# Kernel optimization log

Measured on AMD Instinct MI355X. Metric: run time of the kernel, lower is better.

Reference implementation:

```python
import jax, jax.numpy as jnp
import numpy as np

B, S, D = 4, 2048, 1024
E = 8
H = int(D * 2.5)  # 2560


def setup_inputs() -> dict:
    key = jax.random.key(0)
    ks = jax.random.split(key, 6)
    scale = 0.02
    x = jax.random.normal(ks[0], (B, S, D), dtype=jnp.float32)
    Wr = jax.random.normal(ks[1], (E, D), dtype=jnp.float32) * scale   # router: logits = x @ Wr.T
    Wg = jax.random.normal(ks[2], (E, H, D), dtype=jnp.float32) * scale  # gate proj per expert
    Wu = jax.random.normal(ks[3], (E, H, D), dtype=jnp.float32) * scale  # up proj per expert
    Wd = jax.random.normal(ks[4], (E, D, H), dtype=jnp.float32) * scale  # down proj per expert
    return {"x": x, "Wr": Wr, "Wg": Wg, "Wu": Wu, "Wd": Wd, "top_k": 2}


def reference(x, Wr, Wg, Wu, Wd, top_k):
    num_experts = Wg.shape[0]
    logits = jnp.einsum('bsd,ed->bse', x, Wr)              # [B,S,E]
    probs = jax.nn.softmax(logits, axis=-1)
    k = min(top_k, num_experts)
    topv, topi = jax.lax.top_k(probs, k)                   # [B,S,k]
    out = jnp.zeros_like(x)
    for ei in range(num_experts):
        mask = jnp.any(topi == ei, axis=-1)                # [B,S] bool
        h = jax.nn.silu(jnp.einsum('bsd,hd->bsh', x, Wg[ei])) \
            * jnp.einsum('bsd,hd->bsh', x, Wu[ei])         # [B,S,H]
        ex = jnp.einsum('bsh,dh->bsd', h, Wd[ei])          # [B,S,D]
        w = (probs[..., ei] * mask.astype(x.dtype))[..., None]
        out = out + ex * w
    return (out, logits, probs, topi)
```

## Files before the change

kernel.cpp:

```cpp
#include <hip/hip_runtime.h>

#define T_TOK 8192
#define DD    1024
#define EE    8
#define HH    2560
#define PAIR_CAP (T_TOK*2 + 128)
#define MT_MAX 64
#define NT1   (HH/64)
#define NT2   (DD/128)

typedef __attribute__((ext_vector_type(8))) short bf16x8;
typedef __attribute__((ext_vector_type(4))) float f32x4;

__device__ __forceinline__ unsigned short f2b(float f) {
  union { float f; unsigned u; } v; v.f = f;
  unsigned r = v.u + 0x7FFFu + ((v.u >> 16) & 1u);
  return (unsigned short)(r >> 16);
}

__device__ __forceinline__ void async16(const void* g, void* l) {
  __builtin_amdgcn_global_load_lds(
      (const __attribute__((address_space(1))) unsigned int*)(unsigned long long)g,
      (__attribute__((address_space(3))) unsigned int*)l,
      16, 0, 0);
}

__global__ void zero_f4(float4* p, int n4) {
  int i = blockIdx.x * blockDim.x + threadIdx.x;
  if (i < n4) p[i] = make_float4(0.f, 0.f, 0.f, 0.f);
}

__global__ void zero_ints(int* a, int n) {
  int i = threadIdx.x;
  if (i < n) a[i] = 0;
}

__global__ void conv_bf16(const float* __restrict__ s, unsigned short* __restrict__ d, int n4) {
  int i = blockIdx.x * blockDim.x + threadIdx.x;
  if (i >= n4) return;
  float4 v = ((const float4*)s)[i];
  ushort4 o;
  o.x = f2b(v.x); o.y = f2b(v.y); o.z = f2b(v.z); o.w = f2b(v.w);
  ((ushort4*)d)[i] = o;
}

__global__ __launch_bounds__(256) void router(
    const float* __restrict__ x, const float* __restrict__ Wr,
    float* __restrict__ o_logits, float* __restrict__ o_probs, float* __restrict__ o_topi,
    int* __restrict__ top_e, float* __restrict__ top_p, int* __restrict__ counts)
{
  __shared__ float sWr[EE * DD];
  int tid = threadIdx.x;
  const float4* w4 = (const float4*)Wr;
  float4* s4 = (float4*)sWr;
  for (int i = tid; i < EE * DD / 4; i += 256) s4[i] = w4[i];
  __syncthreads();

  int wv = tid >> 6, lane = tid & 63;
  int t = blockIdx.x * 4 + wv;
  const float* xt = x + (size_t)t * DD;

  float acc[EE];
#pragma unroll
  for (int e = 0; e < EE; e++) acc[e] = 0.f;
  for (int d = lane; d < DD; d += 64) {
    float xv = xt[d];
#pragma unroll
    for (int e = 0; e < EE; e++) acc[e] += xv * sWr[e * DD + d];
  }
#pragma unroll
  for (int e = 0; e < EE; e++) {
#pragma unroll
    for (int off = 32; off; off >>= 1) acc[e] += __shfl_down(acc[e], off);
  }
  if (lane == 0) {
    float mx = acc[0];
#pragma unroll
    for (int e = 1; e < EE; e++) mx = fmaxf(mx, acc[e]);
    float p[EE]; float sum = 0.f;
#pragma unroll
    for (int e = 0; e < EE; e++) { p[e] = __expf(acc[e] - mx); sum += p[e]; }
    float inv = 1.f / sum;
#pragma unroll
    for (int e = 0; e < EE; e++) {
      p[e] *= inv;
      o_logits[(size_t)t * EE + e] = acc[e];
      o_probs [(size_t)t * EE + e] = p[e];
    }
    int i0 = 0;
#pragma unroll
    for (int e = 1; e < EE; e++) if (p[e] > p[i0]) i0 = e;
    int i1 = (i0 == 0) ? 1 : 0;
#pragma unroll
    for (int e = 0; e < EE; e++) if (e != i0 && p[e] > p[i1]) i1 = e;

    o_topi[t * 2 + 0] = (float)i0;
    o_topi[t * 2 + 1] = (float)i1;
    top_e[t * 2 + 0] = i0; top_e[t * 2 + 1] = i1;
    top_p[t * 2 + 0] = p[i0]; top_p[t * 2 + 1] = p[i1];
    atomicAdd(&counts[i0], 1);
    atomicAdd(&counts[i1], 1);
  }
}

__global__ void mk_offsets(const int* __restrict__ counts, int* __restrict__ offsets,
                           int* __restrict__ cursors) {
  if (threadIdx.x == 0) {
    int s = 0;
    for (int e = 0; e < EE; e++) { offsets[e] = s; s += counts[e]; }
  }
  if (threadIdx.x < EE) cursors[threadIdx.x] = 0;
}

__global__ void scatter(const int* __restrict__ top_e, const float* __restrict__ top_p,
                        const int* __restrict__ offsets, int* __restrict__ cursors,
                        int* __restrict__ list, float* __restrict__ wl) {
  int t = blockIdx.x * blockDim.x + threadIdx.x;
  if (t >= T_TOK) return;
#pragma unroll
  for (int k = 0; k < 2; k++) {
    int e = top_e[t * 2 + k];
    int pos = atomicAdd(&cursors[e], 1);
    int dst = offsets[e] + pos;
    list[dst] = t;
    wl[dst] = top_p[t * 2 + k];
  }
}

__global__ __launch_bounds__(256) void gemm_gateup(
    const unsigned short* __restrict__ xb,
    const unsigned short* __restrict__ Wgb,
    const unsigned short* __restrict__ Wub,
    const int* __restrict__ list, const int* __restrict__ offsets,
    const int* __restrict__ counts,
    unsigned short* __restrict__ hbuf)
{
  int bx = blockIdx.x;
  int e = bx / (MT_MAX * NT1);
  int rem = bx - e * (MT_MAX * NT1);
  int mt = rem / NT1;
  int nt = rem - mt * NT1;
  int n_e = counts[e];
  if (mt * 128 >= n_e) return;
  int off_e = offsets[e];

  __shared__ unsigned short sA [128 * 32];
  __shared__ unsigned short sBg[ 64 * 32];
  __shared__ unsigned short sBu[ 64 * 32];

  int tid = threadIdx.x, wv = tid >> 6, lane = tid & 63;
  const unsigned short* wg_e = Wgb + (size_t)e * HH * DD;
  const unsigned short* wu_e = Wub + (size_t)e * HH * DD;

  size_t aBase[2];
#pragma unroll
  for (int i = 0; i < 2; i++) {
    int c = i * 256 + tid;
    int r = c >> 2;
    int idx = mt * 128 + r;
    if (idx >= n_e) idx = n_e - 1;
    int tok = list[off_e + idx];
    aBase[i] = (size_t)tok * DD + (size_t)((c & 3) * 8);
  }
  int rB = tid >> 2;
  size_t bBase = (size_t)(nt * 64 + rB) * DD + (size_t)((tid & 3) * 8);

  f32x4 accg[4][2] = {};
  f32x4 accu[4][2] = {};
  int wm = (wv >> 1) * 64, wn = (wv & 1) * 32;
  unsigned short* ldsA0 = sA  + (wv * 64) * 8;
  unsigned short* ldsA1 = sA  + (256 + wv * 64) * 8;
  unsigned short* ldsBg = sBg + (wv * 64) * 8;
  unsigned short* ldsBu = sBu + (wv * 64) * 8;

  for (int k0 = 0; k0 < DD; k0 += 32) {
    __syncthreads();
    async16(xb + aBase[0] + k0, ldsA0);
    async16(xb + aBase[1] + k0, ldsA1);
    async16(wg_e + bBase + k0, ldsBg);
    async16(wu_e + bBase + k0, ldsBu);
    __syncthreads();

    bf16x8 af[4], bg[2], bu[2];
#pragma unroll
    for (int fi = 0; fi < 4; fi++)
      af[fi] = *(const bf16x8*)&sA[(wm + fi * 16 + (lane & 15)) * 32 + (lane >> 4) * 8];
#pragma unroll
    for (int fj = 0; fj < 2; fj++) {
      bg[fj] = *(const bf16x8*)&sBg[(wn + fj * 16 + (lane & 15)) * 32 + (lane >> 4) * 8];
      bu[fj] = *(const bf16x8*)&sBu[(wn + fj * 16 + (lane & 15)) * 32 + (lane >> 4) * 8];
    }
#pragma unroll
    for (int fi = 0; fi < 4; fi++)
#pragma unroll
      for (int fj = 0; fj < 2; fj++) {
        accg[fi][fj] = __builtin_amdgcn_mfma_f32_16x16x32_bf16(af[fi], bg[fj], accg[fi][fj], 0, 0, 0);
        accu[fi][fj] = __builtin_amdgcn_mfma_f32_16x16x32_bf16(af[fi], bu[fj], accu[fi][fj], 0, 0, 0);
      }
  }

#pragma unroll
  for (int fi = 0; fi < 4; fi++) {
    int mBase = mt * 128 + wm + fi * 16 + ((lane >> 4) << 2);
#pragma unroll
    for (int fj = 0; fj < 2; fj++) {
      int col = nt * 64 + wn + fj * 16 + (lane & 15);
#pragma unroll
      for (int r = 0; r < 4; r++) {
        int m = mBase + r;
        if (m < n_e) {
          float g = accg[fi][fj][r];
          float u = accu[fi][fj][r];
          float hv = g / (1.f + __expf(-g)) * u;
          hbuf[(size_t)(off_e + m) * HH + col] = f2b(hv);
        }
      }
    }
  }
}

__global__ __launch_bounds__(256) void gemm_down(
    const unsigned short* __restrict__ hbuf,
    const unsigned short* __restrict__ Wdb,
    const int* __restrict__ list, const int* __restrict__ offsets,
    const int* __restrict__ counts, const float* __restrict__ wl,
    float* __restrict__ out)
{
  int bx = blockIdx.x;
  int e = bx / (MT_MAX * NT2);
  int rem = bx - e * (MT_MAX * NT2);
  int mt = rem / NT2;
  int nt = rem - mt * NT2;
  int n_e = counts[e];
  if (mt * 128 >= n_e) return;
  int off_e = offsets[e];

  __shared__ unsigned short sA[128 * 32];
  __shared__ unsigned short sB[128 * 32];
  int tid = threadIdx.x, wv = tid >> 6, lane = tid & 63;
  const unsigned short* wd_e = Wdb + (size_t)e * DD * HH;

  size_t aBase[2], bBase[2];
#pragma unroll
  for (int i = 0; i < 2; i++) {
    int c = i * 256 + tid;
    int r = c >> 2;
    aBase[i] = (size_t)(off_e + mt * 128 + r) * HH + (size_t)((c & 3) * 8);
    bBase[i] = (size_t)(nt * 128 + r) * HH + (size_t)((c & 3) * 8);
  }

  f32x4 acc[4][4] = {};
  int wm = (wv >> 1) * 64, wn = (wv & 1) * 64;
  unsigned short* ldsA0 = sA + (wv * 64) * 8;
  unsigned short* ldsA1 = sA + (256 + wv * 64) * 8;
  unsigned short* ldsB0 = sB + (wv * 64) * 8;
  unsigned short* ldsB1 = sB + (256 + wv * 64) * 8;

  for (int k0 = 0; k0 < HH; k0 += 32) {
    __syncthreads();
    async16(hbuf + aBase[0] + k0, ldsA0);
    async16(hbuf + aBase[1] + k0, ldsA1);
    async16(wd_e + bBase[0] + k0, ldsB0);
    async16(wd_e + bBase[1] + k0, ldsB1);
    __syncthreads();

    bf16x8 af[4], bf[4];
#pragma unroll
    for (int f = 0; f < 4; f++) {
      af[f] = *(const bf16x8*)&sA[(wm + f * 16 + (lane & 15)) * 32 + (lane >> 4) * 8];
      bf[f] = *(const bf16x8*)&sB[(wn + f * 16 + (lane & 15)) * 32 + (lane >> 4) * 8];
    }
#pragma unroll
    for (int fi = 0; fi < 4; fi++)
#pragma unroll
      for (int fj = 0; fj < 4; fj++)
        acc[fi][fj] = __builtin_amdgcn_mfma_f32_16x16x32_bf16(af[fi], bf[fj], acc[fi][fj], 0, 0, 0);
  }

#pragma unroll
  for (int fi = 0; fi < 4; fi++) {
    int mBase = mt * 128 + wm + fi * 16 + ((lane >> 4) << 2);
#pragma unroll
    for (int r = 0; r < 4; r++) {
      int m = mBase + r;
      if (m < n_e) {
        int tok   = list[off_e + m];
        float wgt = wl[off_e + m];
        float* orow = out + (size_t)tok * DD + nt * 128 + wn;
#pragma unroll
        for (int fj = 0; fj < 4; fj++)
          atomicAdd(&orow[fj * 16 + (lane & 15)], acc[fi][fj][r] * wgt);
      }
    }
  }
}

extern "C" void kernel_launch(void* const* d_in, const int* in_sizes, int n_in,
                              void* d_out, int out_size, void* d_ws, size_t ws_size,
                              hipStream_t stream) {
  const float* x  = (const float*)d_in[0];
  const float* Wr = (const float*)d_in[1];
  const float* Wg = (const float*)d_in[2];
  const float* Wu = (const float*)d_in[3];
  const float* Wd = (const float*)d_in[4];

  float* out      = (float*)d_out;
  float* o_logits = out + (size_t)T_TOK * DD;
  float* o_probs  = o_logits + (size_t)T_TOK * EE;
  float* o_topi   = o_probs + (size_t)T_TOK * EE;

  char* w = (char*)d_ws;
  auto alloc = [&](size_t bytes) {
    char* p = w;
    w += (bytes + 255) & ~(size_t)255;
    return p;
  };
  unsigned short* Wgb = (unsigned short*)alloc((size_t)EE * HH * DD * 2);
  unsigned short* Wub = (unsigned short*)alloc((size_t)EE * HH * DD * 2);
  unsigned short* Wdb = (unsigned short*)alloc((size_t)EE * DD * HH * 2);
  unsigned short* xb  = (unsigned short*)alloc((size_t)T_TOK * DD * 2);
  unsigned short* hb  = (unsigned short*)alloc((size_t)PAIR_CAP * HH * 2);
  int*   top_e   = (int*)  alloc((size_t)T_TOK * 2 * 4);
  float* top_p   = (float*)alloc((size_t)T_TOK * 2 * 4);
  int*   counts  = (int*)  alloc(64);
  int*   offsets = (int*)  alloc(64);
  int*   cursors = (int*)  alloc(64);
  int*   list    = (int*)  alloc((size_t)PAIR_CAP * 4);
  float* wl      = (float*)alloc((size_t)PAIR_CAP * 4);

  zero_ints<<<1, 64, 0, stream>>>(counts, EE);
  {
    int n4 = T_TOK * DD / 4;
    zero_f4<<<(n4 + 255) / 256, 256, 0, stream>>>((float4*)out, n4);
  }
  {
    int nw4 = EE * HH * DD / 4;
    conv_bf16<<<(nw4 + 255) / 256, 256, 0, stream>>>(Wg, Wgb, nw4);
    conv_bf16<<<(nw4 + 255) / 256, 256, 0, stream>>>(Wu, Wub, nw4);
    conv_bf16<<<(nw4 + 255) / 256, 256, 0, stream>>>(Wd, Wdb, nw4);
    int nx4 = T_TOK * DD / 4;
    conv_bf16<<<(nx4 + 255) / 256, 256, 0, stream>>>(x, xb, nx4);
  }
  router<<<T_TOK / 4, 256, 0, stream>>>(x, Wr, o_logits, o_probs, o_topi, top_e, top_p, counts);
  mk_offsets<<<1, 64, 0, stream>>>(counts, offsets, cursors);
  scatter<<<T_TOK / 256, 256, 0, stream>>>(top_e, top_p, offsets, cursors, list, wl);
  gemm_gateup<<<EE * MT_MAX * NT1, 256, 0, stream>>>(xb, Wgb, Wub, list, offsets, counts, hb);
  gemm_down<<<EE * MT_MAX * NT2, 256, 0, stream>>>(hb, Wdb, list, offsets, counts, wl, out);
}
```

Before: 958.6 us.

## Use K=64 swizzled LDS tiles and replace atomic scatter with a combine pass

Both expert GEMMs now stage 64-wide K tiles in LDS using an XOR swizzle, which halves the number of barrier pairs per K step and is meant to reduce LDS bank conflicts. The down GEMM stores its per-pair results unweighted to a temporary buffer (aliased onto the no-longer-needed bf16 gate weights) instead of issuing float atomics into the output. A new combine kernel does the weighted sum of each token's two expert rows, so the output-zeroing pass can be dropped. This costs an extra round trip through a temporary buffer of pairs by D floats, and it relies on Wgb not being read after gemm_gateup.

```diff
diff --git a/kernel.cpp b/kernel.cpp
--- a/kernel.cpp
+++ b/kernel.cpp
@@ -23,11 +23,6 @@
       (const __attribute__((address_space(1))) unsigned int*)(unsigned long long)g,
       (__attribute__((address_space(3))) unsigned int*)l,
       16, 0, 0);
-}
-
-__global__ void zero_f4(float4* p, int n4) {
-  int i = blockIdx.x * blockDim.x + threadIdx.x;
-  if (i < n4) p[i] = make_float4(0.f, 0.f, 0.f, 0.f);
 }
 
 __global__ void zero_ints(int* a, int n) {
@@ -112,9 +107,9 @@
   if (threadIdx.x < EE) cursors[threadIdx.x] = 0;
 }
 
-__global__ void scatter(const int* __restrict__ top_e, const float* __restrict__ top_p,
+__global__ void scatter(const int* __restrict__ top_e,
                         const int* __restrict__ offsets, int* __restrict__ cursors,
-                        int* __restrict__ list, float* __restrict__ wl) {
+                        int* __restrict__ list, int* __restrict__ slot) {
   int t = blockIdx.x * blockDim.x + threadIdx.x;
   if (t >= T_TOK) return;
 #pragma unroll
@@ -123,7 +118,7 @@
     int pos = atomicAdd(&cursors[e], 1);
     int dst = offsets[e] + pos;
     list[dst] = t;
-    wl[dst] = top_p[t * 2 + k];
+    slot[t * 2 + k] = dst;
   }
 }
 
@@ -144,59 +139,74 @@
   if (mt * 128 >= n_e) return;
   int off_e = offsets[e];
 
-  __shared__ unsigned short sA [128 * 32];
-  __shared__ unsigned short sBg[ 64 * 32];
-  __shared__ unsigned short sBu[ 64 * 32];
+  __shared__ unsigned short sA [128 * 64];
+  __shared__ unsigned short sBg[ 64 * 64];
+  __shared__ unsigned short sBu[ 64 * 64];
 
   int tid = threadIdx.x, wv = tid >> 6, lane = tid & 63;
   const unsigned short* wg_e = Wgb + (size_t)e * HH * DD;
   const unsigned short* wu_e = Wub + (size_t)e * HH * DD;
 
-  size_t aBase[2];
-#pragma unroll
-  for (int i = 0; i < 2; i++) {
+  size_t aBase[4];
+#pragma unroll
+  for (int i = 0; i < 4; i++) {
     int c = i * 256 + tid;
-    int r = c >> 2;
+    int r = c >> 3, j = c & 7;
+    int jj = j ^ (r & 7);
     int idx = mt * 128 + r;
     if (idx >= n_e) idx = n_e - 1;
     int tok = list[off_e + idx];
-    aBase[i] = (size_t)tok * DD + (size_t)((c & 3) * 8);
-  }
-  int rB = tid >> 2;
-  size_t bBase = (size_t)(nt * 64 + rB) * DD + (size_t)((tid & 3) * 8);
+    aBase[i] = (size_t)tok * DD + (size_t)(jj * 8);
+  }
+  size_t bBase[2];
+#pragma unroll
+  for (int i = 0; i < 2; i++) {
+    int c = i * 256 + tid;
+    int r = c >> 3, j = c & 7;
+    int jj = j ^ (r & 7);
+    bBase[i] = (size_t)(nt * 64 + r) * DD + (size_t)(jj * 8);
+  }
 
   f32x4 accg[4][2] = {};
   f32x4 accu[4][2] = {};
   int wm = (wv >> 1) * 64, wn = (wv & 1) * 32;
-  unsigned short* ldsA0 = sA  + (wv * 64) * 8;
-  unsigned short* ldsA1 = sA  + (256 + wv * 64) * 8;
-  unsigned short* ldsBg = sBg + (wv * 64) * 8;
-  unsigned short* ldsBu = sBu + (wv * 64) * 8;
-
-  for (int k0 = 0; k0 < DD; k0 += 32) {
+
+  for (int k0 = 0; k0 < DD; k0 += 64) {
     __syncthreads();
-    async16(xb + aBase[0] + k0, ldsA0);
-    async16(xb + aBase[1] + k0, ldsA1);
-    async16(wg_e + bBase + k0, ldsBg);
-    async16(wu_e + bBase + k0, ldsBu);
+#pragma unroll
+    for (int i = 0; i < 4; i++)
+      async16(xb + aBase[i] + k0, sA + (size_t)(i * 256 + wv * 64) * 8);
+#pragma unroll
+    for (int i = 0; i < 2; i++) {
+      async16(wg_e + bBase[i] + k0, sBg + (size_t)(i * 256 + wv * 64) * 8);
+      async16(wu_e + bBase[i] + k0, sBu + (size_t)(i * 256 + wv * 64) * 8);
+    }
     __syncthreads();
 
-    bf16x8 af[4], bg[2], bu[2];
-#pragma unroll
-    for (int fi = 0; fi < 4; fi++)
-      af[fi] = *(const bf16x8*)&sA[(wm + fi * 16 + (lane & 15)) * 32 + (lane >> 4) * 8];
-#pragma unroll
-    for (int fj = 0; fj < 2; fj++) {
-      bg[fj] = *(const bf16x8*)&sBg[(wn + fj * 16 + (lane & 15)) * 32 + (lane >> 4) * 8];
-      bu[fj] = *(const bf16x8*)&sBu[(wn + fj * 16 + (lane & 15)) * 32 + (lane >> 4) * 8];
-    }
-#pragma unroll
-    for (int fi = 0; fi < 4; fi++)
+#pragma unroll
+    for (int ks = 0; ks < 2; ks++) {
+      bf16x8 af[4], bg[2], bu[2];
+#pragma unroll
+      for (int fi = 0; fi < 4; fi++) {
+        int r = wm + fi * 16 + (lane & 15);
+        int ch = (ks * 4 + (lane >> 4)) ^ (r & 7);
+        af[fi] = *(const bf16x8*)&sA[r * 64 + ch * 8];
+      }
 #pragma unroll
       for (int fj = 0; fj < 2; fj++) {
-        accg[fi][fj] = __builtin_amdgcn_mfma_f32_16x16x32_bf16(af[fi], bg[fj], accg[fi][fj], 0, 0, 0);
-        accu[fi][fj] = __builtin_amdgcn_mfma_f32_16x16x32_bf16(af[fi], bu[fj], accu[fi][fj], 0, 0, 0);
-      }
+        int r = wn + fj * 16 + (lane & 15);
+        int ch = (ks * 4 + (lane >> 4)) ^ (r & 7);
+        bg[fj] = *(const bf16x8*)&sBg[r * 64 + ch * 8];
+        bu[fj] = *(const bf16x8*)&sBu[r * 64 + ch * 8];
+      }
+#pragma unroll
+      for (int fi = 0; fi < 4; fi++)
+#pragma unroll
+        for (int fj = 0; fj < 2; fj++) {
+          accg[fi][fj] = __builtin_amdgcn_mfma_f32_16x16x32_bf16(af[fi], bg[fj], accg[fi][fj], 0, 0, 0);
+          accu[fi][fj] = __builtin_amdgcn_mfma_f32_16x16x32_bf16(af[fi], bu[fj], accu[fi][fj], 0, 0, 0);
+        }
+    }
   }
 
 #pragma unroll
@@ -222,9 +232,9 @@
 __global__ __launch_bounds__(256) void gemm_down(
     const unsigned short* __restrict__ hbuf,
     const unsigned short* __restrict__ Wdb,
-    const int* __restrict__ list, const int* __restrict__ offsets,
-    const int* __restrict__ counts, const float* __restrict__ wl,
-    float* __restrict__ out)
+    const int* __restrict__ offsets,
+    const int* __restrict__ counts,
+    float* __restrict__ tmp)
 {
   int bx = blockIdx.x;
   int e = bx / (MT_MAX * NT2);
@@ -235,46 +245,51 @@
   if (mt * 128 >= n_e) return;
   int off_e = offsets[e];
 
-  __shared__ unsigned short sA[128 * 32];
-  __shared__ unsigned short sB[128 * 32];
+  __shared__ unsigned short sA[128 * 64];
+  __shared__ unsigned short sB[128 * 64];
   int tid = threadIdx.x, wv = tid >> 6, lane = tid & 63;
   const unsigned short* wd_e = Wdb + (size_t)e * DD * HH;
 
-  size_t aBase[2], bBase[2];
-#pragma unroll
-  for (int i = 0; i < 2; i++) {
+  size_t aBase[4], bBase[4];
+#pragma unroll
+  for (int i = 0; i < 4; i++) {
     int c = i * 256 + tid;
-    int r = c >> 2;
-    aBase[i] = (size_t)(off_e + mt * 128 + r) * HH + (size_t)((c & 3) * 8);
-    bBase[i] = (size_t)(nt * 128 + r) * HH + (size_t)((c & 3) * 8);
+    int r = c >> 3, j = c & 7;
+    int jj = j ^ (r & 7);
+    aBase[i] = (size_t)(off_e + mt * 128 + r) * HH + (size_t)(jj * 8);
+    bBase[i] = (size_t)(nt * 128 + r) * HH + (size_t)(jj * 8);
   }
 
   f32x4 acc[4][4] = {};
   int wm = (wv >> 1) * 64, wn = (wv & 1) * 64;
-  unsigned short* ldsA0 = sA + (wv * 64) * 8;
-  unsigned short* ldsA1 = sA + (256 + wv * 64) * 8;
-  unsigned short* ldsB0 = sB + (wv * 64) * 8;
-  unsigned short* ldsB1 = sB + (256 + wv * 64) * 8;
-
-  for (int k0 = 0; k0 < HH; k0 += 32) {
+
+  for (int k0 = 0; k0 < HH; k0 += 64) {
     __syncthreads();
-    async16(hbuf + aBase[0] + k0, ldsA0);
-    async16(hbuf + aBase[1] + k0, ldsA1);
-    async16(wd_e + bBase[0] + k0, ldsB0);
-    async16(wd_e + bBase[1] + k0, ldsB1);
+#pragma unroll
+    for (int i = 0; i < 4; i++) {
+      async16(hbuf + aBase[i] + k0, sA + (size_t)(i * 256 + wv * 64) * 8);
+      async16(wd_e + bBase[i] + k0, sB + (size_t)(i * 256 + wv * 64) * 8);
+    }
     __syncthreads();
 
-    bf16x8 af[4], bf[4];
-#pragma unroll
-    for (int f = 0; f < 4; f++) {
-      af[f] = *(const bf16x8*)&sA[(wm + f * 16 + (lane & 15)) * 32 + (lane >> 4) * 8];
-      bf[f] = *(const bf16x8*)&sB[(wn + f * 16 + (lane & 15)) * 32 + (lane >> 4) * 8];
-    }
-#pragma unroll
-    for (int fi = 0; fi < 4; fi++)
-#pragma unroll
-      for (int fj = 0; fj < 4; fj++)
-        acc[fi][fj] = __builtin_amdgcn_mfma_f32_16x16x32_bf16(af[fi], bf[fj], acc[fi][fj], 0, 0, 0);
+#pragma unroll
+    for (int ks = 0; ks < 2; ks++) {
+      bf16x8 af[4], bf[4];
+#pragma unroll
+      for (int f = 0; f < 4; f++) {
+        int ra = wm + f * 16 + (lane & 15);
+        int ca = (ks * 4 + (lane >> 4)) ^ (ra & 7);
+        af[f] = *(const bf16x8*)&sA[ra * 64 + ca * 8];
+        int rb = wn + f * 16 + (lane & 15);
+        int cb = (ks * 4 + (lane >> 4)) ^ (rb & 7);
+        bf[f] = *(const bf16x8*)&sB[rb * 64 + cb * 8];
+      }
+#pragma unroll
+      for (int fi = 0; fi < 4; fi++)
+#pragma unroll
+        for (int fj = 0; fj < 4; fj++)
+          acc[fi][fj] = __builtin_amdgcn_mfma_f32_16x16x32_bf16(af[fi], bf[fj], acc[fi][fj], 0, 0, 0);
+    }
   }
 
 #pragma unroll
@@ -284,15 +299,30 @@
     for (int r = 0; r < 4; r++) {
       int m = mBase + r;
       if (m < n_e) {
-        int tok   = list[off_e + m];
-        float wgt = wl[off_e + m];
-        float* orow = out + (size_t)tok * DD + nt * 128 + wn;
+        float* orow = tmp + (size_t)(off_e + m) * DD + nt * 128 + wn;
 #pragma unroll
         for (int fj = 0; fj < 4; fj++)
-          atomicAdd(&orow[fj * 16 + (lane & 15)], acc[fi][fj][r] * wgt);
-      }
-    }
-  }
+          orow[fj * 16 + (lane & 15)] = acc[fi][fj][r];
+      }
+    }
+  }
+}
+
+__global__ __launch_bounds__(256) void combine(
+    const float* __restrict__ tmp, const int* __restrict__ slot,
+    const float* __restrict__ top_p, float* __restrict__ out)
+{
+  int t = blockIdx.x, d = threadIdx.x;
+  int s0 = slot[t * 2 + 0], s1 = slot[t * 2 + 1];
+  float p0 = top_p[t * 2 + 0], p1 = top_p[t * 2 + 1];
+  float4 a = ((const float4*)(tmp + (size_t)s0 * DD))[d];
+  float4 b = ((const float4*)(tmp + (size_t)s1 * DD))[d];
+  float4 o;
+  o.x = p0 * a.x + p1 * b.x;
+  o.y = p0 * a.y + p1 * b.y;
+  o.z = p0 * a.z + p1 * b.z;
+  o.w = p0 * a.w + p1 * b.w;
+  ((float4*)(out + (size_t)t * DD))[d] = o;
 }
 
 extern "C" void kernel_launch(void* const* d_in, const int* in_sizes, int n_in,
@@ -326,13 +356,11 @@
   int*   offsets = (int*)  alloc(64);
   int*   cursors = (int*)  alloc(64);
   int*   list    = (int*)  alloc((size_t)PAIR_CAP * 4);
-  float* wl      = (float*)alloc((size_t)PAIR_CAP * 4);
+  int*   slot    = (int*)  alloc((size_t)T_TOK * 2 * 4);
+
+  float* tmp = (float*)Wgb;
 
   zero_ints<<<1, 64, 0, stream>>>(counts, EE);
-  {
-    int n4 = T_TOK * DD / 4;
-    zero_f4<<<(n4 + 255) / 256, 256, 0, stream>>>((float4*)out, n4);
-  }
   {
     int nw4 = EE * HH * DD / 4;
     conv_bf16<<<(nw4 + 255) / 256, 256, 0, stream>>>(Wg, Wgb, nw4);
@@ -343,7 +371,8 @@
   }
   router<<<T_TOK / 4, 256, 0, stream>>>(x, Wr, o_logits, o_probs, o_topi, top_e, top_p, counts);
   mk_offsets<<<1, 64, 0, stream>>>(counts, offsets, cursors);
-  scatter<<<T_TOK / 256, 256, 0, stream>>>(top_e, top_p, offsets, cursors, list, wl);
+  scatter<<<T_TOK / 256, 256, 0, stream>>>(top_e, offsets, cursors, list, slot);
   gemm_gateup<<<EE * MT_MAX * NT1, 256, 0, stream>>>(xb, Wgb, Wub, list, offsets, counts, hb);
-  gemm_down<<<EE * MT_MAX * NT2, 256, 0, stream>>>(hb, Wdb, list, offsets, counts, wl, out);
-}
+  gemm_down<<<EE * MT_MAX * NT2, 256, 0, stream>>>(hb, Wdb, offsets, counts, tmp);
+  combine<<<T_TOK, 256, 0, stream>>>(tmp, slot, top_p, out);
+}
```

Result: no change. 942.6 us (-1.7%).
